# Kernel tuning notes

Measured on AMD Instinct MI355X. Metric: run time of the kernel, lower is better.

## Reference

```python
import jax, jax.numpy as jnp
import numpy as np

UNITS = 256
IN_DIM = 256
OUT_DIM = 10
TOL = 1e-4
MAX_ITER = 50


def setup_inputs() -> dict:
    key = jax.random.key(0)
    ks = jax.random.split(key, 16)
    B = 65536
    s = 1.0 / np.sqrt(UNITS)
    inp = {
        "x": jax.random.normal(ks[0], (B, IN_DIM), dtype=jnp.float32),
        "w_in": jax.random.normal(ks[1], (IN_DIM, UNITS), dtype=jnp.float32) * s,
        "b_in": jax.random.normal(ks[2], (UNITS,), dtype=jnp.float32) * 0.01,
        "w_out": jax.random.normal(ks[3], (UNITS, OUT_DIM), dtype=jnp.float32) * s,
        "b_out": jax.random.normal(ks[4], (OUT_DIM,), dtype=jnp.float32) * 0.01,
    }
    eye = jnp.eye(UNITS, dtype=jnp.float32)
    for i in range(4):
        # well-conditioned (invertible) implicit-layer weight: I + small perturbation
        inp[f"w{i+1}"] = eye + 0.1 * jax.random.normal(ks[5 + 2 * i], (UNITS, UNITS), dtype=jnp.float32) * s
        inp[f"b{i+1}"] = jax.random.normal(ks[6 + 2 * i], (UNITS,), dtype=jnp.float32) * 0.01
    return inp


def newton_block(x, W, b):
    # Solve z @ W = x + tanh(x) + b by Newton iteration with early exit on ||g||.
    c = x + jnp.tanh(x) + b  # [B, n]
    z0 = x
    g0 = z0 @ W - c

    def cond(state):
        z, g, it = state
        return (it < MAX_ITER) & (jnp.linalg.norm(g) >= TOL)

    def body(state):
        z, g, it = state
        # torch.solve(g[:, :, None], W^T.repeat(B,1,1)): shared matrix -> one solve
        z = z - jnp.linalg.solve(W.T, g.T).T
        g = z @ W - c
        return (z, g, it + 1)

    z, _, _ = jax.lax.while_loop(cond, body, (z0, g0, jnp.asarray(0)))
    z = jax.lax.stop_gradient(z)  # torch loop runs under no_grad
    # final differentiable correction (torch: z = z - (z@W - x - tanh(x) - b))
    return z - (z @ W - c)


def reference(x, w_in, b_in, w1, b1, w2, b2, w3, b3, w4, b4, w_out, b_out):
    z = x @ w_in + b_in
    z = newton_block(z, w1, b1)
    z = newton_block(z, w2, b2)
    z = newton_block(z, w3, b3)
    z = newton_block(z, w4, b4)
    logits = z @ w_out + b_out
    return jax.nn.softmax(logits, axis=1)
```

## Files before the change

### kernel.cpp

```cpp
#include <hip/hip_runtime.h>
#include <hip/hip_fp16.h>
#include <math.h>


typedef __attribute__((ext_vector_type(8))) short short8;
typedef __attribute__((ext_vector_type(4))) float f32x4;

__device__ __forceinline__ float tanh_fast(float x) {
#if __has_builtin(__builtin_amdgcn_exp2f)
  float e = __builtin_amdgcn_exp2f(x * 2.8853900817779268f);
#else
  float e = __expf(2.0f * x);
#endif
  return 1.0f - 2.0f * __builtin_amdgcn_rcpf(e + 1.0f);
}
__device__ __forceinline__ unsigned rn_pair16(float v0, float v1) {
  __half2 h = __floats2half2_rn(v0, v1);
  return *reinterpret_cast<unsigned*>(&h);
}
__device__ __forceinline__ unsigned rtz_pair16(float v0, float v1) {
#if __has_builtin(__builtin_amdgcn_cvt_pkrtz)
  typedef __fp16 h2v __attribute__((ext_vector_type(2)));
  h2v h = __builtin_amdgcn_cvt_pkrtz(v0, v1);
  return *reinterpret_cast<unsigned*>(&h);
#else
  return rn_pair16(v0, v1);
#endif
}

__global__ __launch_bounds__(512) void ns_poly_k(
    const float* __restrict__ w1, const float* __restrict__ w2,
    const float* __restrict__ w3, const float* __restrict__ w4,
    const float* __restrict__ w_in, const float* __restrict__ w_out,
    unsigned* __restrict__ pk) {
  const int bid = blockIdx.x;
  const int t = threadIdx.x;
  if (bid >= 256) {
    int idx = (bid - 256) * 512 + t;
    {
      int kc = idx >> 12;
      int nt = (idx >> 8) & 15;
      int lane = (idx >> 2) & 63;
      int d = idx & 3;
      int n = nt * 16 + (lane & 15);
      int kb = kc * 32 + (lane >> 4) * 8 + d * 2;
      pk[idx] = rn_pair16(w_in[kb * 256 + n], w_in[(kb + 1) * 256 + n]);
    }
    int idx2 = idx + 32768;
    if (idx2 < 34816) {
      int r2 = idx2 - 32768;
      int kc = r2 >> 8;
      int lane = (r2 >> 2) & 63;
      int d = r2 & 3;
      int n = lane & 15;
      int kb = kc * 32 + (lane >> 4) * 8 + d * 2;
      float v0 = (n < 10) ? w_out[kb * 10 + n] : 0.0f;
      float v1 = (n < 10) ? w_out[(kb + 1) * 10 + n] : 0.0f;
      pk[5 * 32768 + r2] = rn_pair16(v0, v1);
    }
    return;
  }
  const int m = bid >> 6;
  const int r0 = (bid & 63) * 4;
  const float* __restrict__ W = (m == 0) ? w1 : (m == 1) ? w2 : (m == 2) ? w3 : w4;
  const int tk = t >> 8;
  const int tt = t & 255;
  __shared__ float S[4][256];
  __shared__ float P2[2][4][256];

#pragma unroll
  for (int i = 0; i < 2; ++i) {
    int e = i * 512 + t;
    int r = e >> 8, c = e & 255;
    S[r][c] = (((r0 + r) == c) ? 6.0f : 0.0f) - W[(r0 + r) * 256 + c];
  }
  __syncthreads();

  const float coef[4] = {-15.0f, 20.0f, -15.0f, 6.0f};
#pragma unroll
  for (int step = 0; step < 4; ++step) {
    float acc[4];
#pragma unroll
    for (int r = 0; r < 4; ++r) acc[r] = 0.0f;
    const float* __restrict__ Wk = W + tk * 128 * 256;
    const int kbase = tk * 128;
#pragma unroll 4
    for (int k = 0; k < 128; k += 4) {
      float4 sv[4];
#pragma unroll
      for (int r = 0; r < 4; ++r) sv[r] = *(const float4*)&S[r][kbase + k];
      float wv0 = Wk[(k + 0) * 256 + tt];
      float wv1 = Wk[(k + 1) * 256 + tt];
      float wv2 = Wk[(k + 2) * 256 + tt];
      float wv3 = Wk[(k + 3) * 256 + tt];
#pragma unroll
      for (int r = 0; r < 4; ++r) {
        acc[r] = fmaf(sv[r].x, wv0, acc[r]);
        acc[r] = fmaf(sv[r].y, wv1, acc[r]);
        acc[r] = fmaf(sv[r].z, wv2, acc[r]);
        acc[r] = fmaf(sv[r].w, wv3, acc[r]);
      }
    }
#pragma unroll
    for (int r = 0; r < 4; ++r) P2[tk][r][tt] = acc[r];
    __syncthreads();
    float cdiag = coef[step];
#pragma unroll
    for (int i = 0; i < 2; ++i) {
      int e = i * 512 + t;
      int r = e >> 8, c = e & 255;
      S[r][c] = P2[0][r][c] + P2[1][r][c] + (((r0 + r) == c) ? cdiag : 0.0f);
    }
    __syncthreads();
  }

  const int kc = r0 >> 5;
  const int quad = (r0 >> 3) & 3;
  const int d0 = (r0 & 7) >> 1;
  {
    int q = t;
    int nt = q >> 5;
    int n16 = (q >> 1) & 15;
    int dd = q & 1;
    int n = nt * 16 + n16;
    int lane = quad * 16 + n16;
    unsigned word = rn_pair16(S[2 * dd][n], S[2 * dd + 1][n]);
    pk[(m + 1) * 32768 + kc * 4096 + nt * 256 + lane * 4 + (d0 + dd)] = word;
  }
}

template <int MT>
__global__ __launch_bounds__(256, 4) void fused_k(
    const float* __restrict__ x, const unsigned* __restrict__ pk,
    const float* __restrict__ b_in,
    const float* __restrict__ b1, const float* __restrict__ b2,
    const float* __restrict__ b3, const float* __restrict__ b4,
    const float* __restrict__ b_out, float* __restrict__ out) {
  constexpr int NR = MT * 16;
  __shared__ unsigned short zpl[NR * 256];
  const int t = threadIdx.x;
  const int ln = t & 63;
  const int wv = t >> 6;
  const int quad = ln >> 4;
  const int n16 = ln & 15;
  const int grow0 = blockIdx.x * NR;

#pragma unroll
  for (int i = 0; i < MT * 4; ++i) {
    int e = i * 1024 + t * 4;
    int r = e >> 8, c = e & 255;
    float4 v = *(const float4*)(x + (grow0 + r) * 256 + c);
    int idx = r * 256 + (((c >> 3) ^ (r & 31)) * 8) + (c & 7);
    uint2 zp;
    zp.x = rtz_pair16(v.x, v.y);
    zp.y = rtz_pair16(v.z, v.w);
    *(uint2*)&zpl[idx] = zp;
  }
  __syncthreads();

  const float* bnv[4] = {b1, b2, b3, b4};
  f32x4 acc[MT][4];

  for (int layer = 0; layer < 5; ++layer) {
    const unsigned* pkl = pk + layer * 32768 + wv * 1024 + ln * 4;
#pragma unroll
    for (int mt = 0; mt < MT; ++mt)
#pragma unroll
      for (int nt = 0; nt < 4; ++nt) acc[mt][nt] = (f32x4){0.f, 0.f, 0.f, 0.f};

#pragma unroll 2
    for (int kc = 0; kc < 8; ++kc) {
      short8 wh[4], zf[MT];
      const unsigned* pb = pkl + kc * 4096;
#pragma unroll
      for (int nt = 0; nt < 4; ++nt) wh[nt] = *(const short8*)(pb + nt * 256);
#pragma unroll
      for (int mt = 0; mt < MT; ++mt) {
        int mm = mt * 16 + n16;
        int idx = mm * 256 + (((kc * 4 + quad) ^ (mm & 31)) * 8);
        zf[mt] = *(const short8*)&zpl[idx];
      }
#pragma unroll
      for (int mt = 0; mt < MT; ++mt)
#pragma unroll
        for (int nt = 0; nt < 4; ++nt)
          acc[mt][nt] = __builtin_amdgcn_mfma_f32_16x16x32_f16(wh[nt], zf[mt], acc[mt][nt], 0, 0, 0);
    }
    __syncthreads();

#pragma unroll
    for (int nt = 0; nt < 4; ++nt) {
      int colb = wv * 64 + nt * 16 + quad * 4;
      float4 bi = make_float4(0.f, 0.f, 0.f, 0.f);
      float4 bn4 = bi;
      if (layer == 0) bi = *(const float4*)(b_in + colb);
      if (layer < 4) bn4 = *(const float4*)(bnv[layer] + colb);
#pragma unroll
      for (int mt = 0; mt < MT; ++mt) {
        int row = mt * 16 + n16;
        float v0 = acc[mt][nt][0] + bi.x;
        float v1 = acc[mt][nt][1] + bi.y;
        float v2 = acc[mt][nt][2] + bi.z;
        float v3 = acc[mt][nt][3] + bi.w;
        if (layer < 4) {
          v0 = v0 + tanh_fast(v0) + bn4.x;
          v1 = v1 + tanh_fast(v1) + bn4.y;
          v2 = v2 + tanh_fast(v2) + bn4.z;
          v3 = v3 + tanh_fast(v3) + bn4.w;
        }
        int idx = row * 256 + (((colb >> 3) ^ (row & 31)) * 8) + (colb & 7);
        uint2 zp;
        zp.x = rtz_pair16(v0, v1);
        zp.y = rtz_pair16(v2, v3);
        *(uint2*)&zpl[idx] = zp;
      }
    }
    __syncthreads();
  }

  f32x4 lacc[MT];
#pragma unroll
  for (int mt = 0; mt < MT; ++mt) lacc[mt] = (f32x4){0.f, 0.f, 0.f, 0.f};
  const unsigned* pw = pk + 5 * 32768 + ln * 4;
#pragma unroll
  for (int kk = 0; kk < 2; ++kk) {
    int kc = wv * 2 + kk;
    short8 wh = *(const short8*)(pw + kc * 256);
#pragma unroll
    for (int mt = 0; mt < MT; ++mt) {
      int mm = mt * 16 + n16;
      int idx = mm * 256 + (((kc * 4 + quad) ^ (mm & 31)) * 8);
      short8 zf = *(const short8*)&zpl[idx];
      lacc[mt] = __builtin_amdgcn_mfma_f32_16x16x32_f16(wh, zf, lacc[mt], 0, 0, 0);
    }
  }
  __syncthreads();
  float* pbuf = (float*)zpl;
#pragma unroll
  for (int mt = 0; mt < MT; ++mt) {
    int addr = wv * (NR * 16) + (mt * 16 + n16) * 16 + quad * 4;
    *(f32x4*)&pbuf[addr] = lacc[mt];
  }
  __syncthreads();
  if (t < NR) {
    int r = t;
    float lg[10];
    float mx = -1e30f;
#pragma unroll
    for (int j = 0; j < 10; ++j) {
      float s = b_out[j];
#pragma unroll
      for (int w2 = 0; w2 < 4; ++w2) s += pbuf[w2 * (NR * 16) + r * 16 + j];
      lg[j] = s;
      mx = fmaxf(mx, s);
    }
    float sum = 0.f;
#pragma unroll
    for (int j = 0; j < 10; ++j) {
      lg[j] = __expf(lg[j] - mx);
      sum += lg[j];
    }
    float inv = 1.0f / sum;
    float* op = out + (grow0 + r) * 10;
#pragma unroll
    for (int j = 0; j < 10; ++j) op[j] = lg[j] * inv;
  }
}

extern "C" void kernel_launch(void* const* d_in, const int* in_sizes, int n_in,
                              void* d_out, int out_size, void* d_ws, size_t ws_size,
                              hipStream_t stream) {
  const float* x     = (const float*)d_in[0];
  const float* w_in  = (const float*)d_in[1];
  const float* b_in  = (const float*)d_in[2];
  const float* w_out = (const float*)d_in[3];
  const float* b_out = (const float*)d_in[4];
  const float* w1 = (const float*)d_in[5];
  const float* b1 = (const float*)d_in[6];
  const float* w2 = (const float*)d_in[7];
  const float* b2 = (const float*)d_in[8];
  const float* w3 = (const float*)d_in[9];
  const float* b3 = (const float*)d_in[10];
  const float* w4 = (const float*)d_in[11];
  const float* b4 = (const float*)d_in[12];
  float* out = (float*)d_out;

  unsigned* pk = (unsigned*)d_ws;

  ns_poly_k<<<320, 512, 0, stream>>>(w1, w2, w3, w4, w_in, w_out, pk);
  fused_k<4><<<1024, 256, 0, stream>>>(x, pk, b_in, b1, b2, b3, b4, b_out, out);
}
```

Baseline: 180.5 us.

## Split Newton-Schulz polynomial weight prep into two kernels with shared intermediates

Replaces the single ns_poly_k preprocessing kernel with two kernels. The first computes W^2 and a combined polynomial term G = 20I + 6W^2 - 15W - W^3 and writes both to workspace; the second multiplies W^2 by G, forms the final inverse-approximation matrix and packs it as fp16. This spreads the dependent matrix-product chain across two launches so each block does fewer sequential products, at the cost of an extra launch and extra global-memory round trips. It falls back to the old kernel if the workspace is too small.

```diff
diff --git a/kernel.cpp b/kernel.cpp
--- a/kernel.cpp
+++ b/kernel.cpp
@@ -26,6 +26,205 @@
 #else
   return rn_pair16(v0, v1);
 #endif
+}
+
+
+__global__ __launch_bounds__(512) void ns_poly_a(
+    const float* __restrict__ w1, const float* __restrict__ w2,
+    const float* __restrict__ w3, const float* __restrict__ w4,
+    const float* __restrict__ w_in, const float* __restrict__ w_out,
+    unsigned* __restrict__ pk, float* __restrict__ ws2, float* __restrict__ wsg) {
+  const int bid = blockIdx.x;
+  const int t = threadIdx.x;
+  if (bid >= 256) {
+    int idx = (bid - 256) * 512 + t;
+    {
+      int kc = idx >> 12;
+      int nt = (idx >> 8) & 15;
+      int lane = (idx >> 2) & 63;
+      int d = idx & 3;
+      int n = nt * 16 + (lane & 15);
+      int kb = kc * 32 + (lane >> 4) * 8 + d * 2;
+      pk[idx] = rn_pair16(w_in[kb * 256 + n], w_in[(kb + 1) * 256 + n]);
+    }
+    int idx2 = idx + 32768;
+    if (idx2 < 34816) {
+      int r2 = idx2 - 32768;
+      int kc = r2 >> 8;
+      int lane = (r2 >> 2) & 63;
+      int d = r2 & 3;
+      int n = lane & 15;
+      int kb = kc * 32 + (lane >> 4) * 8 + d * 2;
+      float v0 = (n < 10) ? w_out[kb * 10 + n] : 0.0f;
+      float v1 = (n < 10) ? w_out[(kb + 1) * 10 + n] : 0.0f;
+      pk[5 * 32768 + r2] = rn_pair16(v0, v1);
+    }
+    return;
+  }
+  const int m = bid >> 6;
+  const int r0 = (bid & 63) * 4;
+  const float* __restrict__ W = (m == 0) ? w1 : (m == 1) ? w2 : (m == 2) ? w3 : w4;
+  const int tk = t >> 8;
+  const int tt = t & 255;
+  __shared__ float S[4][256];
+  __shared__ float P2[2][4][256];
+
+#pragma unroll
+  for (int i = 0; i < 2; ++i) {
+    int e = i * 512 + t;
+    int r = e >> 8, c = e & 255;
+    S[r][c] = W[(r0 + r) * 256 + c];
+  }
+  __syncthreads();
+
+  {
+    float acc[4];
+#pragma unroll
+    for (int r = 0; r < 4; ++r) acc[r] = 0.0f;
+    const float* __restrict__ Wk = W + tk * 128 * 256;
+    const int kbase = tk * 128;
+#pragma unroll 4
+    for (int k = 0; k < 128; k += 4) {
+      float4 sv[4];
+#pragma unroll
+      for (int r = 0; r < 4; ++r) sv[r] = *(const float4*)&S[r][kbase + k];
+      float wv0 = Wk[(k + 0) * 256 + tt];
+      float wv1 = Wk[(k + 1) * 256 + tt];
+      float wv2 = Wk[(k + 2) * 256 + tt];
+      float wv3 = Wk[(k + 3) * 256 + tt];
+#pragma unroll
+      for (int r = 0; r < 4; ++r) {
+        acc[r] = fmaf(sv[r].x, wv0, acc[r]);
+        acc[r] = fmaf(sv[r].y, wv1, acc[r]);
+        acc[r] = fmaf(sv[r].z, wv2, acc[r]);
+        acc[r] = fmaf(sv[r].w, wv3, acc[r]);
+      }
+    }
+#pragma unroll
+    for (int r = 0; r < 4; ++r) P2[tk][r][tt] = acc[r];
+    __syncthreads();
+#pragma unroll
+    for (int i = 0; i < 2; ++i) {
+      int e = i * 512 + t;
+      int r = e >> 8, c = e & 255;
+      float v = P2[0][r][c] + P2[1][r][c];
+      S[r][c] = v;
+      ws2[m * 65536 + (r0 + r) * 256 + c] = v;
+    }
+    __syncthreads();
+  }
+
+  {
+    float acc[4];
+#pragma unroll
+    for (int r = 0; r < 4; ++r) acc[r] = 0.0f;
+    const float* __restrict__ Wk = W + tk * 128 * 256;
+    const int kbase = tk * 128;
+#pragma unroll 4
+    for (int k = 0; k < 128; k += 4) {
+      float4 sv[4];
+#pragma unroll
+      for (int r = 0; r < 4; ++r) sv[r] = *(const float4*)&S[r][kbase + k];
+      float wv0 = Wk[(k + 0) * 256 + tt];
+      float wv1 = Wk[(k + 1) * 256 + tt];
+      float wv2 = Wk[(k + 2) * 256 + tt];
+      float wv3 = Wk[(k + 3) * 256 + tt];
+#pragma unroll
+      for (int r = 0; r < 4; ++r) {
+        acc[r] = fmaf(sv[r].x, wv0, acc[r]);
+        acc[r] = fmaf(sv[r].y, wv1, acc[r]);
+        acc[r] = fmaf(sv[r].z, wv2, acc[r]);
+        acc[r] = fmaf(sv[r].w, wv3, acc[r]);
+      }
+    }
+#pragma unroll
+    for (int r = 0; r < 4; ++r) P2[tk][r][tt] = acc[r];
+    __syncthreads();
+#pragma unroll
+    for (int i = 0; i < 2; ++i) {
+      int e = i * 512 + t;
+      int r = e >> 8, c = e & 255;
+      float w3v = P2[0][r][c] + P2[1][r][c];
+      float wv = W[(r0 + r) * 256 + c];
+      float g = fmaf(-15.0f, wv, fmaf(6.0f, S[r][c], -w3v));
+      if ((r0 + r) == c) g += 20.0f;
+      wsg[m * 65536 + (r0 + r) * 256 + c] = g;
+    }
+  }
+}
+
+__global__ __launch_bounds__(512) void ns_poly_b(
+    const float* __restrict__ w1, const float* __restrict__ w2,
+    const float* __restrict__ w3, const float* __restrict__ w4,
+    const float* __restrict__ ws2, const float* __restrict__ wsg,
+    unsigned* __restrict__ pk) {
+  const int bid = blockIdx.x;
+  const int t = threadIdx.x;
+  const int m = bid >> 6;
+  const int r0 = (bid & 63) * 4;
+  const float* __restrict__ W = (m == 0) ? w1 : (m == 1) ? w2 : (m == 2) ? w3 : w4;
+  const int tk = t >> 8;
+  const int tt = t & 255;
+  __shared__ float S[4][256];
+  __shared__ float P2[2][4][256];
+
+#pragma unroll
+  for (int i = 0; i < 2; ++i) {
+    int e = i * 512 + t;
+    int r = e >> 8, c = e & 255;
+    S[r][c] = ws2[m * 65536 + (r0 + r) * 256 + c];
+  }
+  __syncthreads();
+
+  float acc[4];
+#pragma unroll
+  for (int r = 0; r < 4; ++r) acc[r] = 0.0f;
+  const float* __restrict__ Gk = wsg + m * 65536 + tk * 128 * 256;
+  const int kbase = tk * 128;
+#pragma unroll 4
+  for (int k = 0; k < 128; k += 4) {
+    float4 sv[4];
+#pragma unroll
+    for (int r = 0; r < 4; ++r) sv[r] = *(const float4*)&S[r][kbase + k];
+    float gv0 = Gk[(k + 0) * 256 + tt];
+    float gv1 = Gk[(k + 1) * 256 + tt];
+    float gv2 = Gk[(k + 2) * 256 + tt];
+    float gv3 = Gk[(k + 3) * 256 + tt];
+#pragma unroll
+    for (int r = 0; r < 4; ++r) {
+      acc[r] = fmaf(sv[r].x, gv0, acc[r]);
+      acc[r] = fmaf(sv[r].y, gv1, acc[r]);
+      acc[r] = fmaf(sv[r].z, gv2, acc[r]);
+      acc[r] = fmaf(sv[r].w, gv3, acc[r]);
+    }
+  }
+#pragma unroll
+  for (int r = 0; r < 4; ++r) P2[tk][r][tt] = acc[r];
+  __syncthreads();
+#pragma unroll
+  for (int i = 0; i < 2; ++i) {
+    int e = i * 512 + t;
+    int r = e >> 8, c = e & 255;
+    float h = P2[0][r][c] + P2[1][r][c];
+    float p = fmaf(-15.0f, W[(r0 + r) * 256 + c], h);
+    if ((r0 + r) == c) p += 6.0f;
+    S[r][c] = p;
+  }
+  __syncthreads();
+
+  const int kc = r0 >> 5;
+  const int quad = (r0 >> 3) & 3;
+  const int d0 = (r0 & 7) >> 1;
+  {
+    int q = t;
+    int nt = q >> 5;
+    int n16 = (q >> 1) & 15;
+    int dd = q & 1;
+    int n = nt * 16 + n16;
+    int lane = quad * 16 + n16;
+    unsigned word = rn_pair16(S[2 * dd][n], S[2 * dd + 1][n]);
+    pk[(m + 1) * 32768 + kc * 4096 + nt * 256 + lane * 4 + (d0 + dd)] = word;
+  }
 }
 
 __global__ __launch_bounds__(512) void ns_poly_k(
@@ -286,7 +485,17 @@
   float* out = (float*)d_out;
 
   unsigned* pk = (unsigned*)d_ws;
-
-  ns_poly_k<<<320, 512, 0, stream>>>(w1, w2, w3, w4, w_in, w_out, pk);
+  const size_t pk_dw = 165888;
+  const size_t mat_dw = 4 * 256 * 256;
+  const size_t need_bytes = (pk_dw + 2 * mat_dw) * 4;
+
+  if (ws_size >= need_bytes) {
+    float* ws2 = (float*)d_ws + pk_dw;
+    float* wsg = (float*)d_ws + pk_dw + mat_dw;
+    ns_poly_a<<<320, 512, 0, stream>>>(w1, w2, w3, w4, w_in, w_out, pk, ws2, wsg);
+    ns_poly_b<<<256, 512, 0, stream>>>(w1, w2, w3, w4, ws2, wsg, pk);
+  } else {
+    ns_poly_k<<<320, 512, 0, stream>>>(w1, w2, w3, w4, w_in, w_out, pk);
+  }
   fused_k<4><<<1024, 256, 0, stream>>>(x, pk, b_in, b1, b2, b3, b4, b_out, out);
 }
```

New measurement: 185.7 us. 2.9% more time.
